# Performance work log

Hardware: AMD Instinct MI355X
Metric: run time of the kernel (lower is better)

The kernel has to match this reference:

```python
import jax, jax.numpy as jnp
import numpy as np

N_MEMORY = 128
INPUT_LEN = 512
OUTPUT_LEN = 256
N_FRAMES = 65536


def setup_inputs() -> dict:
    key = jax.random.key(0)
    k1, k2, k3, k4, k5 = jax.random.split(key, 5)
    return {
        "inputs": jax.random.normal(k1, (INPUT_LEN, N_FRAMES), dtype=jnp.float32),
        "W1": jax.random.normal(k2, (2 * N_MEMORY, INPUT_LEN), dtype=jnp.float32) * 0.05,
        "B1": jax.random.normal(k3, (2 * N_MEMORY, 1), dtype=jnp.float32) * 0.05,
        "W2": jax.random.normal(k4, (OUTPUT_LEN, N_MEMORY), dtype=jnp.float32) * 0.05,
        "B2": jax.random.normal(k5, (OUTPUT_LEN, 1), dtype=jnp.float32) * 0.05,
    }


def reference(inputs, W1, B1, W2, B2):
    # h: (2M, T)
    h = jax.nn.sigmoid(jnp.matmul(W1, inputs) + B1)
    M = W1.shape[0] // 2
    left, right = h[:M], h[M:]          # each (M, T)
    prod = left * right                  # gate product, (M, T)

    # Linear recurrence: u_0 = 0; u_t = prod[:, t-1] * u_{t-1} + (1 - left[:, t-1])
    # Affine pairs for t = 1..T-1, time-major: (T-1, M)
    a = prod[:, :-1].T
    b = (1.0 - left[:, :-1]).T

    def combine(c1, c2):
        a1, b1 = c1
        a2, b2 = c2
        return a1 * a2, a2 * b1 + b2

    _, bb = jax.lax.associative_scan(combine, (a, b))
    # u_0 = 0 => u_t = bb_t; prepend the zero initial state as column 0
    z = jnp.concatenate([jnp.zeros((M, 1), dtype=inputs.dtype), bb.T], axis=1)  # (M, T)

    out = 1.0 - jax.nn.sigmoid(jnp.matmul(W2, z) + B2)  # (output_len, T)
    return out
```

## Files before the change

kernel.cpp:

```cpp
#include <hip/hip_runtime.h>

typedef unsigned short u16;
typedef short bf16x8 __attribute__((ext_vector_type(8)));
typedef float f32x4 __attribute__((ext_vector_type(4)));

#define NF 65536
#define GCH 512

__device__ __forceinline__ float sigm(float x){ return 1.0f/(1.0f+__expf(-x)); }

__device__ __forceinline__ u16 f2bf(float f){
  union { float f; unsigned u; } v; v.f = f;
  unsigned r = (v.u + 0x7fffu + ((v.u >> 16) & 1u)) >> 16;
  return (u16)r;
}

#define AS1(p) ((const __attribute__((address_space(1))) unsigned int*)(p))
#define AS3(p) ((__attribute__((address_space(3))) unsigned int*)(p))

__global__ __launch_bounds__(256) void k_prep(const float* __restrict__ W1, const float* __restrict__ W2,
                                              u16* __restrict__ W1f, u16* __restrict__ W2f){
  int idx = blockIdx.x*256 + threadIdx.x;
  {
    int j  = idx & 7;
    int L  = (idx >> 3) & 63;
    int ks = (idx >> 9) & 1;
    int rt = (idx >> 10) & 15;
    int ck = idx >> 14;
    int row = 16*rt + (L & 15);
    int k   = ck*64 + ks*32 + ((L >> 4) << 3) + j;
    W1f[idx] = f2bf(W1[row*512 + k]);
  }
  if (idx < 32768){
    int j  = idx & 7;
    int L  = (idx >> 3) & 63;
    int ks = (idx >> 9) & 3;
    int rt = idx >> 11;
    int row = 16*rt + (L & 15);
    int m   = ks*32 + ((L >> 4) << 3) + j;
    W2f[idx] = f2bf(W2[row*128 + m]);
  }
}

__global__ __launch_bounds__(256, 2) void k_gemm1(const float* __restrict__ x,
        const u16* __restrict__ W1f, const float* __restrict__ B1,
        float* __restrict__ Aa, float* __restrict__ Bb,
        float* __restrict__ Ac, float* __restrict__ Bc){
  __shared__ __align__(16) float ls[8192];
  __shared__ __align__(16) u16  xs[8192];
  const int tid = threadIdx.x;
  const int wv = tid >> 6, L = tid & 63;
  const int q = L >> 4, ln = L & 15;
  const int g = blockIdx.x;
  const int F0 = g * 128;
  const int rt0 = 2*wv;
  const bf16x8* W1f8 = (const bf16x8*)W1f;

  f32x4 acc[4][8];
  #pragma unroll
  for (int a=0;a<4;a++)
    #pragma unroll
    for (int c=0;c<8;c++) acc[a][c] = (f32x4){0.f,0.f,0.f,0.f};

  for (int ck=0; ck<8; ++ck){
    #pragma unroll
    for (int i=0;i<8;i++){
      int seg = wv*8 + i;
      __builtin_amdgcn_global_load_lds(
        AS1(x + (size_t)(ck*64 + seg*2 + (L>>5))*NF + F0 + (L&31)*4),
        AS3(ls + seg*256), 16, 0, 0);
    }
    bf16x8 af[2][4];
    #pragma unroll
    for (int ks=0;ks<2;ks++){
      af[ks][0] = W1f8[ck*2048 + ((rt0  )*2+ks)*64 + L];
      af[ks][1] = W1f8[ck*2048 + ((rt0+1)*2+ks)*64 + L];
      af[ks][2] = W1f8[ck*2048 + ((rt0+8)*2+ks)*64 + L];
      af[ks][3] = W1f8[ck*2048 + ((rt0+9)*2+ks)*64 + L];
    }
    __syncthreads();
    #pragma unroll
    for (int i=0;i<4;i++){
      int s    = tid + 256*i;
      int lns  = s & 15;
      int codd = (s >> 4) & 1;
      int qs   = (s >> 5) & 3;
      int chi  = (s >> 7) & 3;
      int kss  = (s >> 9) & 1;
      int cc   = chi*2 + codd;
      const float* rp = ls + (kss*32 + qs*8)*128 + cc*16 + lns;
      unsigned u[8];
      #pragma unroll
      for (int j=0;j<8;j++) u[j] = f2bf(rp[j*128]);
      uint4 pk;
      pk.x = u[0] | (u[1]<<16); pk.y = u[2] | (u[3]<<16);
      pk.z = u[4] | (u[5]<<16); pk.w = u[6] | (u[7]<<16);
      *(uint4*)(xs + ((cc*2+kss)*64 + qs*16 + lns)*8) = pk;
    }
    __syncthreads();
    #pragma unroll
    for (int ks=0; ks<2; ++ks){
      #pragma unroll
      for (int c=0;c<8;c++){
        bf16x8 bf = ((const bf16x8*)xs)[(c*2+ks)*64 + L];
        acc[0][c] = __builtin_amdgcn_mfma_f32_16x16x32_bf16(af[ks][0], bf, acc[0][c], 0,0,0);
        acc[1][c] = __builtin_amdgcn_mfma_f32_16x16x32_bf16(af[ks][1], bf, acc[1][c], 0,0,0);
        acc[2][c] = __builtin_amdgcn_mfma_f32_16x16x32_bf16(af[ks][2], bf, acc[2][c], 0,0,0);
        acc[3][c] = __builtin_amdgcn_mfma_f32_16x16x32_bf16(af[ks][3], bf, acc[3][c], 0,0,0);
      }
    }
  }
  __syncthreads();
  #pragma unroll
  for (int pr=0; pr<2; ++pr){
    int mb = 32*wv + 16*pr + 4*q;
    float bl[4], br[4];
    #pragma unroll
    for (int r=0;r<4;r++){ bl[r] = B1[mb+r]; br[r] = B1[mb+128+r]; }
    float RA[4], RB[4];
    #pragma unroll
    for (int c=0;c<8;c++){
      int t = F0 + 16*c + ln;
      f32x4 Lv = acc[pr][c], Rv = acc[pr+2][c];
      float a4[4], b4[4];
      #pragma unroll
      for (int r=0;r<4;r++){
        float le = sigm(Lv[r] + bl[r]);
        float ri = sigm(Rv[r] + br[r]);
        a4[r] = le*ri; b4[r] = 1.0f - le;
      }
      *(float4*)(Aa + (size_t)t*128 + mb) = make_float4(a4[0],a4[1],a4[2],a4[3]);
      *(float4*)(Bb + (size_t)t*128 + mb) = make_float4(b4[0],b4[1],b4[2],b4[3]);
      #pragma unroll
      for (int r=0;r<4;r++){
        float As = a4[r], Bs = b4[r];
        #pragma unroll
        for (int d=1; d<16; d<<=1){
          float Ap = __shfl_xor(As, d);
          float Bp = __shfl_xor(Bs, d);
          Bs = (ln & d) ? fmaf(As, Bp, Bs) : fmaf(Ap, Bs, Bp);
          As *= Ap;
        }
        if (c == 0){ RA[r] = As; RB[r] = Bs; }
        else       { RB[r] = fmaf(As, RB[r], Bs); RA[r] *= As; }
      }
    }
    if (ln == 0){
      #pragma unroll
      for (int r=0;r<4;r++){
        Ac[g*128 + mb + r] = RA[r];
        Bc[g*128 + mb + r] = RB[r];
      }
    }
  }
}

__global__ __launch_bounds__(512, 2) void k_apply(const float* __restrict__ Aa, const float* __restrict__ Bb,
        const float* __restrict__ Ac, const float* __restrict__ Bc,
        const u16* __restrict__ W2f, const float* __restrict__ B2,
        float* __restrict__ out){
  __shared__ __align__(16) u16 zf[16384];
  __shared__ float sA[4][128], sB[4][128];
  const int tid = threadIdx.x;
  const int g = blockIdx.x, T0 = g*128;
  const int m = tid & 127, s4 = tid >> 7;

  float vpref;
  {
    int c0 = s4*128, c1 = c0 + 128; if (c1 > g) c1 = g;
    float A = 1.f, B = 0.f;
    #pragma unroll 4
    for (int c = c0; c < c1; ++c){
      float a = Ac[c*128 + m], b = Bc[c*128 + m];
      B = fmaf(a, B, b);
      A *= a;
    }
    sA[s4][m] = A; sB[s4][m] = B;
    __syncthreads();
    float v = 0.f;
    #pragma unroll
    for (int s2=0; s2<4; ++s2) v = fmaf(sA[s2][m], v, sB[s2][m]);
    vpref = v;
    __syncthreads();
  }

  {
    const float* ap = Aa + (size_t)(T0 + s4*32)*128 + m;
    const float* bp = Bb + (size_t)(T0 + s4*32)*128 + m;
    float areg[32], breg[32];
    #pragma unroll
    for (int i=0;i<32;i++){ areg[i] = ap[(size_t)i*128]; breg[i] = bp[(size_t)i*128]; }
    float A = 1.f, Bv = 0.f;
    #pragma unroll
    for (int i=0;i<32;i++){ Bv = fmaf(areg[i], Bv, breg[i]); A *= areg[i]; }
    sA[s4][m] = A; sB[s4][m] = Bv;
    __syncthreads();
    float v = vpref;
    for (int s2=0; s2<s4; ++s2) v = fmaf(sA[s2][m], v, sB[s2][m]);
    const int base_m = (m>>5)*512 + ((m>>3)&3)*128 + (m&7);
    #pragma unroll
    for (int i=0;i<32;i++){
      int t = s4*32 + i;
      zf[base_m + (t>>4)*2048 + (t&15)*8] = f2bf(v);
      v = fmaf(areg[i], v, breg[i]);
    }
  }
  __syncthreads();

  const int wv = tid >> 6, L = tid & 63;
  const int q = L >> 4, ln = L & 15;
  f32x4 acc[2][8];
  #pragma unroll
  for (int a=0;a<2;a++)
    #pragma unroll
    for (int c=0;c<8;c++) acc[a][c] = (f32x4){0.f,0.f,0.f,0.f};

  #pragma unroll
  for (int ks=0; ks<4; ++ks){
    bf16x8 af0 = ((const bf16x8*)W2f)[((2*wv  )*4+ks)*64 + L];
    bf16x8 af1 = ((const bf16x8*)W2f)[((2*wv+1)*4+ks)*64 + L];
    #pragma unroll
    for (int c=0;c<8;c++){
      bf16x8 bf = ((const bf16x8*)zf)[(c*4+ks)*64 + L];
      acc[0][c] = __builtin_amdgcn_mfma_f32_16x16x32_bf16(af0, bf, acc[0][c], 0,0,0);
      acc[1][c] = __builtin_amdgcn_mfma_f32_16x16x32_bf16(af1, bf, acc[1][c], 0,0,0);
    }
  }

  #pragma unroll
  for (int rs=0;rs<2;rs++){
    int rowb = (2*wv+rs)*16 + q*4;
    float b2[4];
    #pragma unroll
    for (int r=0;r<4;r++) b2[r] = B2[rowb+r];
    #pragma unroll
    for (int c=0;c<8;c++){
      int t = T0 + 16*c + ln;
      #pragma unroll
      for (int r=0;r<4;r++)
        out[(size_t)(rowb+r)*NF + t] = sigm(-(acc[rs][c][r] + b2[r]));
    }
  }
}

extern "C" void kernel_launch(void* const* d_in, const int* in_sizes, int n_in,
                              void* d_out, int out_size, void* d_ws, size_t ws_size,
                              hipStream_t stream) {
  const float* x  = (const float*)d_in[0];
  const float* W1 = (const float*)d_in[1];
  const float* B1 = (const float*)d_in[2];
  const float* W2 = (const float*)d_in[3];
  const float* B2 = (const float*)d_in[4];
  float* out = (float*)d_out;

  u16*   W1f = (u16*)d_ws;
  u16*   W2f = W1f + 131072;
  float* Aa  = (float*)d_ws + 81920;
  float* Bb  = Aa + (size_t)NF*128;
  float* Ac  = Bb + (size_t)NF*128;
  float* Bc  = Ac + (size_t)GCH*128;

  k_prep <<<512, 256, 0, stream>>>(W1, W2, W1f, W2f);
  k_gemm1<<<512, 256, 0, stream>>>(x, W1f, B1, Aa, Bb, Ac, Bc);
  k_apply<<<GCH, 512, 0, stream>>>(Aa, Bb, Ac, Bc, W2f, B2, out);
}
```

Measured before the change: 299.4 us.

## Halve frame tiles, double-buffer x loads, add hierarchical carry scan kernel

Shrinks the per-block frame tile from 128 to 64 so both GEMM kernels launch 1024 blocks with higher occupancy. The input staging in k_gemm1 is double-buffered so the next chunk's global-to-LDS load overlaps the current chunk's bf16 conversion and MFMA work. A new k_scan kernel reduces chunk carries into 16 macro-carries, so each k_apply block folds at most 64 chunk carries plus up to 16 macro carries instead of scanning up to 512 serially. The cost is an extra kernel launch and a smaller tile per block, which gives less reuse of the W1 fragments.

```diff
diff --git a/kernel.cpp b/kernel.cpp
--- a/kernel.cpp
+++ b/kernel.cpp
@@ -5,7 +5,8 @@
 typedef float f32x4 __attribute__((ext_vector_type(4)));
 
 #define NF 65536
-#define GCH 512
+#define NSC 1024
+#define NMAC 16
 
 __device__ __forceinline__ float sigm(float x){ return 1.0f/(1.0f+__expf(-x)); }
 
@@ -42,33 +43,44 @@
   }
 }
 
-__global__ __launch_bounds__(256, 2) void k_gemm1(const float* __restrict__ x,
+__global__ __launch_bounds__(256, 4) void k_gemm1(const float* __restrict__ x,
         const u16* __restrict__ W1f, const float* __restrict__ B1,
         float* __restrict__ Aa, float* __restrict__ Bb,
         float* __restrict__ Ac, float* __restrict__ Bc){
   __shared__ __align__(16) float ls[8192];
-  __shared__ __align__(16) u16  xs[8192];
+  __shared__ __align__(16) u16  xs[4096];
   const int tid = threadIdx.x;
   const int wv = tid >> 6, L = tid & 63;
   const int q = L >> 4, ln = L & 15;
   const int g = blockIdx.x;
-  const int F0 = g * 128;
+  const int F0 = g * 64;
   const int rt0 = 2*wv;
   const bf16x8* W1f8 = (const bf16x8*)W1f;
 
-  f32x4 acc[4][8];
+  f32x4 acc[4][4];
   #pragma unroll
   for (int a=0;a<4;a++)
     #pragma unroll
-    for (int c=0;c<8;c++) acc[a][c] = (f32x4){0.f,0.f,0.f,0.f};
+    for (int c=0;c<4;c++) acc[a][c] = (f32x4){0.f,0.f,0.f,0.f};
+
+  #pragma unroll
+  for (int i=0;i<4;i++){
+    int seg = wv*4 + i;
+    __builtin_amdgcn_global_load_lds(
+      AS1(x + (size_t)(seg*4 + q)*NF + F0 + ln*4),
+      AS3(ls + seg*256), 16, 0, 0);
+  }
 
   for (int ck=0; ck<8; ++ck){
-    #pragma unroll
-    for (int i=0;i<8;i++){
-      int seg = wv*8 + i;
-      __builtin_amdgcn_global_load_lds(
-        AS1(x + (size_t)(ck*64 + seg*2 + (L>>5))*NF + F0 + (L&31)*4),
-        AS3(ls + seg*256), 16, 0, 0);
+    __syncthreads();
+    if (ck < 7){
+      #pragma unroll
+      for (int i=0;i<4;i++){
+        int seg = wv*4 + i;
+        __builtin_amdgcn_global_load_lds(
+          AS1(x + (size_t)((ck+1)*64 + seg*4 + q)*NF + F0 + ln*4),
+          AS3(ls + ((ck+1)&1)*4096 + seg*256), 16, 0, 0);
+      }
     }
     bf16x8 af[2][4];
     #pragma unroll
@@ -78,30 +90,30 @@
       af[ks][2] = W1f8[ck*2048 + ((rt0+8)*2+ks)*64 + L];
       af[ks][3] = W1f8[ck*2048 + ((rt0+9)*2+ks)*64 + L];
     }
-    __syncthreads();
-    #pragma unroll
-    for (int i=0;i<4;i++){
-      int s    = tid + 256*i;
-      int lns  = s & 15;
-      int codd = (s >> 4) & 1;
-      int qs   = (s >> 5) & 3;
-      int chi  = (s >> 7) & 3;
-      int kss  = (s >> 9) & 1;
-      int cc   = chi*2 + codd;
-      const float* rp = ls + (kss*32 + qs*8)*128 + cc*16 + lns;
-      unsigned u[8];
-      #pragma unroll
-      for (int j=0;j<8;j++) u[j] = f2bf(rp[j*128]);
-      uint4 pk;
-      pk.x = u[0] | (u[1]<<16); pk.y = u[2] | (u[3]<<16);
-      pk.z = u[4] | (u[5]<<16); pk.w = u[6] | (u[7]<<16);
-      *(uint4*)(xs + ((cc*2+kss)*64 + qs*16 + lns)*8) = pk;
+    {
+      const float* lsb = ls + (ck&1)*4096;
+      #pragma unroll
+      for (int i=0;i<2;i++){
+        int s    = tid + 256*i;
+        int lns  = s & 15;
+        int cc   = (s >> 4) & 3;
+        int qs   = (s >> 6) & 3;
+        int kss  = (s >> 8) & 1;
+        const float* rp = lsb + (kss*32 + qs*8)*64 + cc*16 + lns;
+        unsigned u[8];
+        #pragma unroll
+        for (int j=0;j<8;j++) u[j] = f2bf(rp[j*64]);
+        uint4 pk;
+        pk.x = u[0] | (u[1]<<16); pk.y = u[2] | (u[3]<<16);
+        pk.z = u[4] | (u[5]<<16); pk.w = u[6] | (u[7]<<16);
+        *(uint4*)(xs + ((cc*2+kss)*64 + qs*16 + lns)*8) = pk;
+      }
     }
     __syncthreads();
     #pragma unroll
     for (int ks=0; ks<2; ++ks){
       #pragma unroll
-      for (int c=0;c<8;c++){
+      for (int c=0;c<4;c++){
         bf16x8 bf = ((const bf16x8*)xs)[(c*2+ks)*64 + L];
         acc[0][c] = __builtin_amdgcn_mfma_f32_16x16x32_bf16(af[ks][0], bf, acc[0][c], 0,0,0);
         acc[1][c] = __builtin_amdgcn_mfma_f32_16x16x32_bf16(af[ks][1], bf, acc[1][c], 0,0,0);
@@ -110,23 +122,26 @@
       }
     }
   }
-  __syncthreads();
-  #pragma unroll
-  for (int pr=0; pr<2; ++pr){
+
+  float bl[2][4], br[2][4], RA[2][4], RB[2][4];
+  #pragma unroll
+  for (int pr=0;pr<2;pr++){
     int mb = 32*wv + 16*pr + 4*q;
-    float bl[4], br[4];
-    #pragma unroll
-    for (int r=0;r<4;r++){ bl[r] = B1[mb+r]; br[r] = B1[mb+128+r]; }
-    float RA[4], RB[4];
-    #pragma unroll
-    for (int c=0;c<8;c++){
-      int t = F0 + 16*c + ln;
+    #pragma unroll
+    for (int r=0;r<4;r++){ bl[pr][r] = B1[mb+r]; br[pr][r] = B1[mb+128+r]; }
+  }
+  #pragma unroll
+  for (int c=0;c<4;c++){
+    int t = F0 + 16*c + ln;
+    #pragma unroll
+    for (int pr=0;pr<2;pr++){
+      int mb = 32*wv + 16*pr + 4*q;
       f32x4 Lv = acc[pr][c], Rv = acc[pr+2][c];
       float a4[4], b4[4];
       #pragma unroll
       for (int r=0;r<4;r++){
-        float le = sigm(Lv[r] + bl[r]);
-        float ri = sigm(Rv[r] + br[r]);
+        float le = sigm(Lv[r] + bl[pr][r]);
+        float ri = sigm(Rv[r] + br[pr][r]);
         a4[r] = le*ri; b4[r] = 1.0f - le;
       }
       *(float4*)(Aa + (size_t)t*128 + mb) = make_float4(a4[0],a4[1],a4[2],a4[3]);
@@ -141,46 +156,73 @@
           Bs = (ln & d) ? fmaf(As, Bp, Bs) : fmaf(Ap, Bs, Bp);
           As *= Ap;
         }
-        if (c == 0){ RA[r] = As; RB[r] = Bs; }
-        else       { RB[r] = fmaf(As, RB[r], Bs); RA[r] *= As; }
-      }
-    }
-    if (ln == 0){
+        if (c == 0){ RA[pr][r] = As; RB[pr][r] = Bs; }
+        else       { RB[pr][r] = fmaf(As, RB[pr][r], Bs); RA[pr][r] *= As; }
+      }
+    }
+  }
+  if (ln == 0){
+    #pragma unroll
+    for (int pr=0;pr<2;pr++){
+      int mb = 32*wv + 16*pr + 4*q;
       #pragma unroll
       for (int r=0;r<4;r++){
-        Ac[g*128 + mb + r] = RA[r];
-        Bc[g*128 + mb + r] = RB[r];
-      }
-    }
-  }
-}
-
-__global__ __launch_bounds__(512, 2) void k_apply(const float* __restrict__ Aa, const float* __restrict__ Bb,
+        Ac[g*128 + mb + r] = RA[pr][r];
+        Bc[g*128 + mb + r] = RB[pr][r];
+      }
+    }
+  }
+}
+
+__global__ __launch_bounds__(256) void k_scan(const float* __restrict__ Ac, const float* __restrict__ Bc,
+                                              float* __restrict__ MtA, float* __restrict__ MtB){
+  __shared__ float sA[2][128], sB[2][128];
+  const int j = blockIdx.x;
+  const int m = threadIdx.x & 127, s4 = threadIdx.x >> 7;
+  const int c0 = j*64 + s4*32;
+  float A = 1.f, B = 0.f;
+  #pragma unroll 8
+  for (int i=0;i<32;i++){
+    float a = Ac[(c0+i)*128 + m], b = Bc[(c0+i)*128 + m];
+    B = fmaf(a, B, b);
+    A *= a;
+  }
+  sA[s4][m] = A; sB[s4][m] = B;
+  __syncthreads();
+  if (s4 == 0){
+    MtA[j*128+m] = sA[1][m] * sA[0][m];
+    MtB[j*128+m] = fmaf(sA[1][m], sB[0][m], sB[1][m]);
+  }
+}
+
+__global__ __launch_bounds__(256, 4) void k_apply(const float* __restrict__ Aa, const float* __restrict__ Bb,
         const float* __restrict__ Ac, const float* __restrict__ Bc,
+        const float* __restrict__ MtA, const float* __restrict__ MtB,
         const u16* __restrict__ W2f, const float* __restrict__ B2,
         float* __restrict__ out){
-  __shared__ __align__(16) u16 zf[16384];
-  __shared__ float sA[4][128], sB[4][128];
+  __shared__ __align__(16) u16 zf[8192];
+  __shared__ float sA[2][128], sB[2][128];
   const int tid = threadIdx.x;
-  const int g = blockIdx.x, T0 = g*128;
+  const int g = blockIdx.x, T0 = g*64;
   const int m = tid & 127, s4 = tid >> 7;
 
-  float vpref;
+  float vg;
   {
-    int c0 = s4*128, c1 = c0 + 128; if (c1 > g) c1 = g;
+    const int j = g >> 6, r0 = j << 6, n = g & 63;
+    int c0 = r0 + s4*32, c1 = r0 + n; if (c1 > c0+32) c1 = c0+32;
     float A = 1.f, B = 0.f;
-    #pragma unroll 4
     for (int c = c0; c < c1; ++c){
       float a = Ac[c*128 + m], b = Bc[c*128 + m];
       B = fmaf(a, B, b);
       A *= a;
     }
     sA[s4][m] = A; sB[s4][m] = B;
-    __syncthreads();
     float v = 0.f;
-    #pragma unroll
-    for (int s2=0; s2<4; ++s2) v = fmaf(sA[s2][m], v, sB[s2][m]);
-    vpref = v;
+    for (int jj=0; jj<j; ++jj) v = fmaf(MtA[jj*128+m], v, MtB[jj*128+m]);
+    __syncthreads();
+    v = fmaf(sA[0][m], v, sB[0][m]);
+    v = fmaf(sA[1][m], v, sB[1][m]);
+    vg = v;
     __syncthreads();
   }
 
@@ -195,8 +237,8 @@
     for (int i=0;i<32;i++){ Bv = fmaf(areg[i], Bv, breg[i]); A *= areg[i]; }
     sA[s4][m] = A; sB[s4][m] = Bv;
     __syncthreads();
-    float v = vpref;
-    for (int s2=0; s2<s4; ++s2) v = fmaf(sA[s2][m], v, sB[s2][m]);
+    float v = vg;
+    if (s4 == 1) v = fmaf(sA[0][m], v, sB[0][m]);
     const int base_m = (m>>5)*512 + ((m>>3)&3)*128 + (m&7);
     #pragma unroll
     for (int i=0;i<32;i++){
@@ -209,36 +251,37 @@
 
   const int wv = tid >> 6, L = tid & 63;
   const int q = L >> 4, ln = L & 15;
-  f32x4 acc[2][8];
-  #pragma unroll
-  for (int a=0;a<2;a++)
-    #pragma unroll
-    for (int c=0;c<8;c++) acc[a][c] = (f32x4){0.f,0.f,0.f,0.f};
+  f32x4 acc[4][4];
+  #pragma unroll
+  for (int a=0;a<4;a++)
+    #pragma unroll
+    for (int c=0;c<4;c++) acc[a][c] = (f32x4){0.f,0.f,0.f,0.f};
 
   #pragma unroll
   for (int ks=0; ks<4; ++ks){
-    bf16x8 af0 = ((const bf16x8*)W2f)[((2*wv  )*4+ks)*64 + L];
-    bf16x8 af1 = ((const bf16x8*)W2f)[((2*wv+1)*4+ks)*64 + L];
-    #pragma unroll
-    for (int c=0;c<8;c++){
+    bf16x8 af[4];
+    #pragma unroll
+    for (int a=0;a<4;a++) af[a] = ((const bf16x8*)W2f)[((4*wv+a)*4+ks)*64 + L];
+    #pragma unroll
+    for (int c=0;c<4;c++){
       bf16x8 bf = ((const bf16x8*)zf)[(c*4+ks)*64 + L];
-      acc[0][c] = __builtin_amdgcn_mfma_f32_16x16x32_bf16(af0, bf, acc[0][c], 0,0,0);
-      acc[1][c] = __builtin_amdgcn_mfma_f32_16x16x32_bf16(af1, bf, acc[1][c], 0,0,0);
-    }
-  }
-
-  #pragma unroll
-  for (int rs=0;rs<2;rs++){
-    int rowb = (2*wv+rs)*16 + q*4;
+      #pragma unroll
+      for (int a=0;a<4;a++)
+        acc[a][c] = __builtin_amdgcn_mfma_f32_16x16x32_bf16(af[a], bf, acc[a][c], 0,0,0);
+    }
+  }
+
+  #pragma unroll
+  for (int a=0;a<4;a++){
+    int rowb = (4*wv+a)*16 + q*4;
     float b2[4];
     #pragma unroll
     for (int r=0;r<4;r++) b2[r] = B2[rowb+r];
     #pragma unroll
-    for (int c=0;c<8;c++){
-      int t = T0 + 16*c + ln;
-      #pragma unroll
-      for (int r=0;r<4;r++)
-        out[(size_t)(rowb+r)*NF + t] = sigm(-(acc[rs][c][r] + b2[r]));
+    for (int r=0;r<4;r++){
+      #pragma unroll
+      for (int c=0;c<4;c++)
+        out[(size_t)(rowb+r)*NF + T0 + 16*c + ln] = sigm(-(acc[a][c][r] + b2[r]));
     }
   }
 }
@@ -258,9 +301,12 @@
   float* Aa  = (float*)d_ws + 81920;
   float* Bb  = Aa + (size_t)NF*128;
   float* Ac  = Bb + (size_t)NF*128;
-  float* Bc  = Ac + (size_t)GCH*128;
+  float* Bc  = Ac + (size_t)NSC*128;
+  float* MtA = Bc + (size_t)NSC*128;
+  float* MtB = MtA + (size_t)NMAC*128;
 
   k_prep <<<512, 256, 0, stream>>>(W1, W2, W1f, W2f);
-  k_gemm1<<<512, 256, 0, stream>>>(x, W1f, B1, Aa, Bb, Ac, Bc);
-  k_apply<<<GCH, 512, 0, stream>>>(Aa, Bb, Ac, Bc, W2f, B2, out);
-}
+  k_gemm1<<<NSC, 256, 0, stream>>>(x, W1f, B1, Aa, Bb, Ac, Bc);
+  k_scan <<<NMAC, 256, 0, stream>>>(Ac, Bc, MtA, MtB);
+  k_apply<<<NSC, 256, 0, stream>>>(Aa, Bb, Ac, Bc, MtA, MtB, W2f, B2, out);
+}
```

Result: faster. 287.2 us (-4.1%).
